# Kernel tuning notes

Measured on AMD Instinct MI355X. Metric: run time of the kernel, lower is better.

The kernel has to match this reference:

```python
import jax, jax.numpy as jnp
import numpy as np


def setup_inputs() -> dict:
    key = jax.random.key(0)
    k = jax.random.split(key, 5)
    C, Cb = 128, 64
    x = jax.random.normal(k[0], (8, C, 64, 64), dtype=jnp.float32)
    s_in = 1.0 / np.sqrt(C)
    s_b = 1.0 / np.sqrt(Cb)
    w_theta = jax.random.normal(k[1], (Cb, C), dtype=jnp.float32) * s_in
    w_phi = jax.random.normal(k[2], (Cb, C), dtype=jnp.float32) * s_in
    w_g = jax.random.normal(k[3], (Cb, C), dtype=jnp.float32) * s_in
    w_last = jax.random.normal(k[4], (C, Cb), dtype=jnp.float32) * s_b
    return {"x": x, "w_theta": w_theta, "w_phi": w_phi, "w_g": w_g, "w_last": w_last}


def reference(x, w_theta, w_phi, w_g, w_last):
    B, C, H, W = x.shape
    xf = x.reshape(B, C, H * W)            # [B, C, N]
    theta = jnp.einsum('kc,bcn->bkn', w_theta, xf)   # [B, Cb, N]
    phi = jnp.einsum('kc,bcn->bkn', w_phi, xf)       # [B, Cb, N]
    g = jnp.einsum('kc,bcn->bkn', w_g, xf)           # [B, Cb, N]
    # attention over spatial positions: [B, N, N]
    attn = jax.nn.softmax(jnp.einsum('bkn,bkm->bnm', theta, phi), axis=-1)
    y = jnp.einsum('bnm,bkm->bkn', attn, g)          # [B, Cb, N]
    out = jnp.einsum('ck,bkn->bcn', w_last, y).reshape(B, C, H, W)
    return out + x
```

## Files before the change

### kernel.cpp

```cpp
#include <hip/hip_runtime.h>
#include <stdint.h>

typedef _Float16 h8v __attribute__((ext_vector_type(8)));
typedef _Float16 h4v __attribute__((ext_vector_type(4)));
typedef float f4v __attribute__((ext_vector_type(4)));
typedef _Float16 f16;

#define NB 8
#define CC 128
#define CB 64
#define NN 4096
#define L2E 1.4426950408889634f

#define GLD(gp, lp) __builtin_amdgcn_global_load_lds( \
    (const __attribute__((address_space(1))) void*)(gp), \
    (__attribute__((address_space(3))) void*)(lp), 16, 0, 0)

#define WAITV2() asm volatile("s_waitcnt vmcnt(2)" ::: "memory")
#define WAITV0() asm volatile("s_waitcnt vmcnt(0)" ::: "memory")
#define WAITL0() asm volatile("s_waitcnt lgkmcnt(0)" ::: "memory")

__global__ __launch_bounds__(256) void pack_w(
    const float* __restrict__ wth, const float* __restrict__ wph,
    const float* __restrict__ wg,  const float* __restrict__ wl,
    f16* __restrict__ wthp, f16* __restrict__ wphp,
    f16* __restrict__ wgp,  f16* __restrict__ wlp)
{
    const int t = blockIdx.x * 256 + threadIdx.x;
    for (int i = t; i < 8192; i += 2048){
        const int j = i & 7, lane = (i >> 3) & 63, kc = (i >> 9) & 3, ks = i >> 11;
        const int row = ks * 16 + (lane & 15);
        const int col = kc * 32 + ((lane >> 4) & 3) * 8 + j;
        wthp[i] = (f16)(wth[row * CC + col] * L2E);
        wphp[i] = (f16)(wph[row * CC + col]);
        wgp [i] = (f16)(wg [row * CC + col]);
    }
    for (int i = t; i < 8192; i += 2048){
        const int j = i & 7, lane = (i >> 3) & 63, kc = (i >> 9) & 1, cs = i >> 10;
        const int row = cs * 16 + (lane & 15);
        const int col = kc * 32 + ((lane >> 4) & 3) * 8 + j;
        wlp[i] = (f16)(wl[row * CB + col]);
    }
}

__global__ __launch_bounds__(256) void proj_kernel(
    const float* __restrict__ x, const f16* __restrict__ wthp,
    const f16* __restrict__ wphp, const f16* __restrict__ wgp,
    f16* __restrict__ thetaT, f16* __restrict__ phiT, f16* __restrict__ gbuf)
{
    __shared__ __align__(16) f16 xT[64][136];
    __shared__ __align__(16) f16 rep[4][16 * 72];
    const int b  = blockIdx.x & 7;
    const int n0 = (blockIdx.x >> 3) << 6;
    const int t  = threadIdx.x;

    #pragma unroll
    for (int i = 0; i < 8; i++){
        int v  = t + 256 * i;
        int c  = v >> 4;
        int j0 = (v & 15) << 2;
        const f4v xv = *(const f4v*)&x[((size_t)(b * CC + c)) * NN + n0 + j0];
        #pragma unroll
        for (int jj = 0; jj < 4; jj++) xT[j0 + jj][c] = (f16)xv[jj];
    }
    __syncthreads();

    const int w = t >> 6, lane = t & 63, quad = lane >> 4, l15 = lane & 15;
    const int rrow = lane >> 3, rcol = (lane & 7) * 8;

    h8v bx[4];
    #pragma unroll
    for (int kc = 0; kc < 4; kc++)
        bx[kc] = *(const h8v*)&xT[w * 16 + l15][kc * 32 + quad * 8];

    #pragma unroll
    for (int m3 = 0; m3 < 2; m3++){
        const f16* WP = (m3 == 0) ? wthp : wphp;
        f16* OUT      = (m3 == 0) ? thetaT : phiT;
        for (int ks = 0; ks < 4; ks++){
            f4v acc = {0.f, 0.f, 0.f, 0.f};
            #pragma unroll
            for (int kc = 0; kc < 4; kc++){
                const h8v af = *(const h8v*)&WP[(ks * 4 + kc) * 512 + lane * 8];
                acc = __builtin_amdgcn_mfma_f32_16x16x32_f16(af, bx[kc], acc, 0, 0, 0);
            }
            h4v pv;
            #pragma unroll
            for (int r = 0; r < 4; r++) pv[r] = (f16)acc[r];
            *(h4v*)&rep[w][l15 * 72 + ks * 16 + quad * 4] = pv;
        }
        #pragma unroll
        for (int j = 0; j < 2; j++){
            const h8v vv = *(const h8v*)&rep[w][(rrow + 8 * j) * 72 + rcol];
            *(h8v*)&OUT[((size_t)(b * NN + n0 + w * 16 + rrow + 8 * j)) * CB + rcol] = vv;
        }
    }

    h8v bw[4];
    #pragma unroll
    for (int kc = 0; kc < 4; kc++)
        bw[kc] = *(const h8v*)&wgp[(w * 4 + kc) * 512 + lane * 8];
    for (int ns = 0; ns < 4; ns++){
        f4v acc = {0.f, 0.f, 0.f, 0.f};
        #pragma unroll
        for (int kc = 0; kc < 4; kc++){
            const h8v af = *(const h8v*)&xT[ns * 16 + l15][kc * 32 + quad * 8];
            acc = __builtin_amdgcn_mfma_f32_16x16x32_f16(af, bw[kc], acc, 0, 0, 0);
        }
        h4v pv;
        #pragma unroll
        for (int r = 0; r < 4; r++) pv[r] = (f16)acc[r];
        *(h4v*)&rep[w][l15 * 72 + ns * 16 + quad * 4] = pv;
    }
    #pragma unroll
    for (int j = 0; j < 2; j++){
        const h8v vv = *(const h8v*)&rep[w][(rrow + 8 * j) * 72 + rcol];
        *(h8v*)&gbuf[((size_t)(b * CB + w * 16 + rrow + 8 * j)) * NN + n0 + rcol] = vv;
    }
}

__global__ __launch_bounds__(512, 4) void attn_kernel(
    const f16* __restrict__ thetaT, const f16* __restrict__ phiT,
    const f16* __restrict__ gbuf, const f16* __restrict__ wlp,
    const float* __restrict__ x, float* __restrict__ out)
{
    __shared__ __align__(16) char SM[59392];
    f16*   const PH  = (f16*)SM;
    f16*   const GG  = (f16*)(SM + 24576);
    f16*   const PLD = (f16*)(SM + 49152);
    float* const MG  = (float*)SM;
    float* const ML  = (float*)(SM + 17408);
    float* const FO  = (float*)SM;
    f16*   const YY  = (f16*)(SM + 36864);

    const int b  = blockIdx.x & 7;
    const int q0 = (blockIdx.x >> 3) << 6;
    const int t  = threadIdx.x;
    const int w  = t >> 6;
    const int lane = t & 63, quad = lane >> 4, l15 = lane & 15;
    const int wq = w & 3;
    const int h  = w >> 2;
    const int n0 = q0 + wq * 16;

    const size_t trow = ((size_t)(b * NN + n0 + l15)) * CB;
    const h8v a0 = *(const h8v*)&thetaT[trow + quad * 8];
    const h8v a1 = *(const h8v*)&thetaT[trow + 32 + quad * 8];

    const int seg  = w * 2;
    const int tsel = seg >> 3;
    const int kind = (seg >> 2) & 1;
    const int qa   = seg & 3;
    const f16* sA;  const f16* sB;  size_t adv;
    if (kind == 0){
        const int row = qa * 8 + (lane >> 3);
        const int gr  = (lane & 7) ^ (lane >> 3);
        sA = phiT + ((size_t)(b * NN + tsel * 32 + row)) * CB + gr * 8;
        sB = sA + (size_t)8 * CB;
        adv = (size_t)64 * CB;
    } else {
        const int row = qa * 16 + (lane >> 2);
        const int gr  = (lane & 3) ^ ((lane >> 2) & 3);
        sA = gbuf + ((size_t)(b * CB + row)) * NN + tsel * 32 + gr * 8;
        sB = sA + (size_t)16 * NN;
        adv = 64;
    }
    f16* const dBase = (kind == 0) ? PH : GG;
    const int dOff = qa * 512;

    const int so0 = (quad ^ (l15 & 7)) * 8;
    const int so1 = so0 ^ 32;
    const int go  = (quad ^ (l15 & 3)) * 8;

    {
        f16* d0 = dBase + (0 + tsel) * 2048 + dOff;
        GLD(sA, d0);  GLD(sB, d0 + 512);
        f16* d1 = dBase + (2 + tsel) * 2048 + dOff;
        GLD(sA + adv, d1);  GLD(sB + adv, d1 + 512);
    }
    const f16* pA = sA + 2 * adv;
    const f16* pB = sB + 2 * adv;

    float mrun = -1e30f, lrun = 0.f;
    const f4v zf = {0.f, 0.f, 0.f, 0.f};
    f4v o[4];
    #pragma unroll
    for (int tt = 0; tt < 4; tt++) o[tt] = zf;

    f16* const PW = PLD + w * 640;

    int rc = 0;
    int rs = 2;
    for (int m = 0; m < 64; m++){
        if (m < 63) WAITV2(); else WAITV0();
        WAITL0();
        __builtin_amdgcn_s_barrier();
        asm volatile("" ::: "memory");
        if (m < 62){
            f16* d = dBase + (2 * rs + tsel) * 2048 + dOff;
            GLD(pA, d);  GLD(pB, d + 512);
            pA += adv;   pB += adv;
        }
        const int ct = 2 * rc + h;
        const f16* phc = PH + ct * 2048;
        const f16* ggc = GG + ct * 2048;

        f4v s[2];
        __builtin_amdgcn_s_setprio(1);
        #pragma unroll
        for (int tt = 0; tt < 2; tt++){
            const f16* pr = phc + (tt * 16 + l15) * 64;
            const h8v pb0 = *(const h8v*)(pr + so0);
            const h8v pb1 = *(const h8v*)(pr + so1);
            f4v sv = zf;
            sv = __builtin_amdgcn_mfma_f32_16x16x32_f16(pb0, a0, sv, 0, 0, 0);
            sv = __builtin_amdgcn_mfma_f32_16x16x32_f16(pb1, a1, sv, 0, 0, 0);
            s[tt] = sv;
        }
        __builtin_amdgcn_s_setprio(0);

        float smax = fmaxf(fmaxf(s[0][0], s[0][1]), fmaxf(s[0][2], s[0][3]));
        smax = fmaxf(smax, fmaxf(fmaxf(s[1][0], s[1][1]), fmaxf(s[1][2], s[1][3])));
        smax = fmaxf(smax, __shfl_xor(smax, 16));
        smax = fmaxf(smax, __shfl_xor(smax, 32));

        if (__any(smax - mrun > 8.f)){
            const float mn = fmaxf(mrun, smax);
            const float alpha = __builtin_amdgcn_exp2f(mrun - mn);
            mrun = mn;
            lrun *= alpha;
            #pragma unroll
            for (int tt = 0; tt < 4; tt++)
                #pragma unroll
                for (int r = 0; r < 4; r++)
                    o[tt][r] *= alpha;
        }

        float lsum = 0.f;
        #pragma unroll
        for (int tt = 0; tt < 2; tt++){
            h4v pv;
            #pragma unroll
            for (int r = 0; r < 4; r++){
                float p = __builtin_amdgcn_exp2f(s[tt][r] - mrun);
                lsum += p;
                pv[r] = (f16)p;
            }
            *(h4v*)&PW[l15 * 40 + tt * 16 + quad * 4] = pv;
        }
        lrun += lsum;

        const h8v pa = *(const h8v*)&PW[l15 * 40 + quad * 8];

        __builtin_amdgcn_s_setprio(1);
        #pragma unroll
        for (int tt2 = 0; tt2 < 4; tt2++){
            const h8v gb = *(const h8v*)(ggc + (tt2 * 16 + l15) * 32 + go);
            o[tt2] = __builtin_amdgcn_mfma_f32_16x16x32_f16(gb, pa, o[tt2], 0, 0, 0);
        }
        __builtin_amdgcn_s_setprio(0);

        rc = (rc == 2) ? 0 : rc + 1;
        rs = (rs == 2) ? 0 : rs + 1;
    }

    lrun += __shfl_xor(lrun, 16);
    lrun += __shfl_xor(lrun, 32);

    __syncthreads();

    if (h == 1){
        #pragma unroll
        for (int tt2 = 0; tt2 < 4; tt2++)
            *(f4v*)&MG[wq * 1088 + l15 * 68 + tt2 * 16 + quad * 4] = o[tt2];
        if (lane < 16){
            ML[wq * 32 + lane * 2 + 0] = mrun;
            ML[wq * 32 + lane * 2 + 1] = lrun;
        }
    }
    __syncthreads();

    if (h == 0){
        const float m4 = ML[wq * 32 + l15 * 2 + 0];
        const float l4 = ML[wq * 32 + l15 * 2 + 1];
        const float M  = fmaxf(mrun, m4);
        const float e0 = __builtin_amdgcn_exp2f(mrun - M);
        const float e1 = __builtin_amdgcn_exp2f(m4 - M);
        const float inv = 1.0f / (lrun * e0 + l4 * e1);
        #pragma unroll
        for (int tt2 = 0; tt2 < 4; tt2++){
            const f4v o4 = *(const f4v*)&MG[wq * 1088 + l15 * 68 + tt2 * 16 + quad * 4];
            h4v yv;
            #pragma unroll
            for (int r = 0; r < 4; r++)
                yv[r] = (f16)((o[tt2][r] * e0 + o4[r] * e1) * inv);
            *(h4v*)&YY[(wq * 16 + l15) * 72 + tt2 * 16 + quad * 4] = yv;
        }
    }
    __syncthreads();

    const h8v yB0 = *(const h8v*)&YY[(wq * 16 + l15) * 72 + quad * 8];
    const h8v yB1 = *(const h8v*)&YY[(wq * 16 + l15) * 72 + 32 + quad * 8];
    #pragma unroll
    for (int ci = 0; ci < 4; ci++){
        const int cs = h * 4 + ci;
        const h8v wa0 = *(const h8v*)&wlp[(cs * 2 + 0) * 512 + lane * 8];
        const h8v wa1 = *(const h8v*)&wlp[(cs * 2 + 1) * 512 + lane * 8];
        f4v acc = zf;
        acc = __builtin_amdgcn_mfma_f32_16x16x32_f16(wa0, yB0, acc, 0, 0, 0);
        acc = __builtin_amdgcn_mfma_f32_16x16x32_f16(wa1, yB1, acc, 0, 0, 0);
        #pragma unroll
        for (int r = 0; r < 4; r++)
            FO[(cs * 16 + quad * 4 + r) * 68 + wq * 16 + l15] = acc[r];
    }
    __syncthreads();

    #pragma unroll
    for (int i = 0; i < 4; i++){
        const int row = i * 32 + (t >> 4);
        const int nf  = (t & 15) * 4;
        const f4v v = *(const f4v*)&FO[row * 68 + nf];
        const size_t idx = ((size_t)(b * CC + row)) * NN + q0 + nf;
        const f4v xv = *(const f4v*)&x[idx];
        f4v ov;
        #pragma unroll
        for (int r = 0; r < 4; r++) ov[r] = v[r] + xv[r];
        *(f4v*)&out[idx] = ov;
    }
}

extern "C" void kernel_launch(void* const* d_in, const int* in_sizes, int n_in,
                              void* d_out, int out_size, void* d_ws, size_t ws_size,
                              hipStream_t stream)
{
    const float* x   = (const float*)d_in[0];
    const float* wth = (const float*)d_in[1];
    const float* wph = (const float*)d_in[2];
    const float* wg  = (const float*)d_in[3];
    const float* wl  = (const float*)d_in[4];
    float* out = (float*)d_out;

    f16* thetaT = (f16*)d_ws;
    f16* phiT   = thetaT + (size_t)NB * NN * CB;
    f16* gbuf   = phiT   + (size_t)NB * NN * CB;
    f16* wthp   = gbuf   + (size_t)NB * NN * CB;
    f16* wphp   = wthp + 8192;
    f16* wgp    = wphp + 8192;
    f16* wlp    = wgp  + 8192;

    pack_w<<<8, 256, 0, stream>>>(wth, wph, wg, wl, wthp, wphp, wgp, wlp);
    proj_kernel<<<NB * 64, 256, 0, stream>>>(x, wthp, wphp, wgp, thetaT, phiT, gbuf);
    attn_kernel<<<NB * 64, 512, 0, stream>>>(thetaT, phiT, gbuf, wlp, x, out);
}
```

Measured before the change: 150.7 us.

## Load g operand directly from global into registers and drop weight-pack kernel

The attention kernel no longer stages g tiles in shared memory. Each wave now loads its g MFMA operands directly from global memory into registers, and the shared-memory pipeline carries only phi in 128-key tiles, halving the loop trip count. The P·G MFMA is split into two halves so the P transpose buffer can be reused. The separate pack_w launch is removed, and weights are converted from fp32 to fp16 inline inside the projection and attention kernels. This trades shared-memory traffic and one launch for uncoalesced, strided global g loads whose latency is less hidden, plus redundant weight conversion in every block.

```diff
diff --git a/kernel.cpp b/kernel.cpp
--- a/kernel.cpp
+++ b/kernel.cpp
@@ -20,32 +20,9 @@
 #define WAITV0() asm volatile("s_waitcnt vmcnt(0)" ::: "memory")
 #define WAITL0() asm volatile("s_waitcnt lgkmcnt(0)" ::: "memory")
 
-__global__ __launch_bounds__(256) void pack_w(
-    const float* __restrict__ wth, const float* __restrict__ wph,
-    const float* __restrict__ wg,  const float* __restrict__ wl,
-    f16* __restrict__ wthp, f16* __restrict__ wphp,
-    f16* __restrict__ wgp,  f16* __restrict__ wlp)
-{
-    const int t = blockIdx.x * 256 + threadIdx.x;
-    for (int i = t; i < 8192; i += 2048){
-        const int j = i & 7, lane = (i >> 3) & 63, kc = (i >> 9) & 3, ks = i >> 11;
-        const int row = ks * 16 + (lane & 15);
-        const int col = kc * 32 + ((lane >> 4) & 3) * 8 + j;
-        wthp[i] = (f16)(wth[row * CC + col] * L2E);
-        wphp[i] = (f16)(wph[row * CC + col]);
-        wgp [i] = (f16)(wg [row * CC + col]);
-    }
-    for (int i = t; i < 8192; i += 2048){
-        const int j = i & 7, lane = (i >> 3) & 63, kc = (i >> 9) & 1, cs = i >> 10;
-        const int row = cs * 16 + (lane & 15);
-        const int col = kc * 32 + ((lane >> 4) & 3) * 8 + j;
-        wlp[i] = (f16)(wl[row * CB + col]);
-    }
-}
-
 __global__ __launch_bounds__(256) void proj_kernel(
-    const float* __restrict__ x, const f16* __restrict__ wthp,
-    const f16* __restrict__ wphp, const f16* __restrict__ wgp,
+    const float* __restrict__ x, const float* __restrict__ wth,
+    const float* __restrict__ wph, const float* __restrict__ wg,
     f16* __restrict__ thetaT, f16* __restrict__ phiT, f16* __restrict__ gbuf)
 {
     __shared__ __align__(16) f16 xT[64][136];
@@ -75,13 +52,22 @@
 
     #pragma unroll
     for (int m3 = 0; m3 < 2; m3++){
-        const f16* WP = (m3 == 0) ? wthp : wphp;
-        f16* OUT      = (m3 == 0) ? thetaT : phiT;
+        const float* WF = (m3 == 0) ? wth : wph;
+        const float sc = (m3 == 0) ? L2E : 1.0f;
+        f16* OUT       = (m3 == 0) ? thetaT : phiT;
         for (int ks = 0; ks < 4; ks++){
             f4v acc = {0.f, 0.f, 0.f, 0.f};
             #pragma unroll
             for (int kc = 0; kc < 4; kc++){
-                const h8v af = *(const h8v*)&WP[(ks * 4 + kc) * 512 + lane * 8];
+                const float* wr = WF + (ks * 16 + l15) * CC + kc * 32 + quad * 8;
+                const f4v wa = *(const f4v*)wr;
+                const f4v wb = *(const f4v*)(wr + 4);
+                h8v af;
+                #pragma unroll
+                for (int j = 0; j < 4; j++){
+                    af[j]     = (f16)(wa[j] * sc);
+                    af[4 + j] = (f16)(wb[j] * sc);
+                }
                 acc = __builtin_amdgcn_mfma_f32_16x16x32_f16(af, bx[kc], acc, 0, 0, 0);
             }
             h4v pv;
@@ -98,8 +84,16 @@
 
     h8v bw[4];
     #pragma unroll
-    for (int kc = 0; kc < 4; kc++)
-        bw[kc] = *(const h8v*)&wgp[(w * 4 + kc) * 512 + lane * 8];
+    for (int kc = 0; kc < 4; kc++){
+        const float* wr = wg + (w * 16 + l15) * CC + kc * 32 + quad * 8;
+        const f4v wa = *(const f4v*)wr;
+        const f4v wb = *(const f4v*)(wr + 4);
+        #pragma unroll
+        for (int j = 0; j < 4; j++){
+            bw[kc][j]     = (f16)wa[j];
+            bw[kc][4 + j] = (f16)wb[j];
+        }
+    }
     for (int ns = 0; ns < 4; ns++){
         f4v acc = {0.f, 0.f, 0.f, 0.f};
         #pragma unroll
@@ -121,12 +115,11 @@
 
 __global__ __launch_bounds__(512, 4) void attn_kernel(
     const f16* __restrict__ thetaT, const f16* __restrict__ phiT,
-    const f16* __restrict__ gbuf, const f16* __restrict__ wlp,
+    const f16* __restrict__ gbuf, const float* __restrict__ wl,
     const float* __restrict__ x, float* __restrict__ out)
 {
     __shared__ __align__(16) char SM[59392];
     f16*   const PH  = (f16*)SM;
-    f16*   const GG  = (f16*)(SM + 24576);
     f16*   const PLD = (f16*)(SM + 49152);
     float* const MG  = (float*)SM;
     float* const ML  = (float*)(SM + 17408);
@@ -146,39 +139,23 @@
     const h8v a0 = *(const h8v*)&thetaT[trow + quad * 8];
     const h8v a1 = *(const h8v*)&thetaT[trow + 32 + quad * 8];
 
-    const int seg  = w * 2;
-    const int tsel = seg >> 3;
-    const int kind = (seg >> 2) & 1;
-    const int qa   = seg & 3;
-    const f16* sA;  const f16* sB;  size_t adv;
-    if (kind == 0){
-        const int row = qa * 8 + (lane >> 3);
-        const int gr  = (lane & 7) ^ (lane >> 3);
-        sA = phiT + ((size_t)(b * NN + tsel * 32 + row)) * CB + gr * 8;
-        sB = sA + (size_t)8 * CB;
-        adv = (size_t)64 * CB;
-    } else {
-        const int row = qa * 16 + (lane >> 2);
-        const int gr  = (lane & 3) ^ ((lane >> 2) & 3);
-        sA = gbuf + ((size_t)(b * CB + row)) * NN + tsel * 32 + gr * 8;
-        sB = sA + (size_t)16 * NN;
-        adv = 64;
-    }
-    f16* const dBase = (kind == 0) ? PH : GG;
-    const int dOff = qa * 512;
+    const int r0 = t >> 3;
+    const int gr = (t & 7) ^ (r0 & 7);
+    const f16* pS = phiT + ((size_t)(b * NN + r0)) * CB + gr * 8;
+    const size_t SADV = (size_t)128 * CB;
 
     const int so0 = (quad ^ (l15 & 7)) * 8;
     const int so1 = so0 ^ 32;
-    const int go  = (quad ^ (l15 & 3)) * 8;
+
+    const f16* pgm = gbuf + ((size_t)(b * CB + l15)) * NN + 64 * h + quad * 8;
 
     {
-        f16* d0 = dBase + (0 + tsel) * 2048 + dOff;
-        GLD(sA, d0);  GLD(sB, d0 + 512);
-        f16* d1 = dBase + (2 + tsel) * 2048 + dOff;
-        GLD(sA + adv, d1);  GLD(sB + adv, d1 + 512);
-    }
-    const f16* pA = sA + 2 * adv;
-    const f16* pB = sB + 2 * adv;
+        GLD(pS,            PH + t * 8);
+        GLD(pS + 64 * CB,  PH + t * 8 + 4096);
+        GLD(pS + SADV,           PH + 8192 + t * 8);
+        GLD(pS + SADV + 64 * CB, PH + 8192 + t * 8 + 4096);
+        pS += 2 * SADV;
+    }
 
     float mrun = -1e30f, lrun = 0.f;
     const f4v zf = {0.f, 0.f, 0.f, 0.f};
@@ -190,24 +167,36 @@
 
     int rc = 0;
     int rs = 2;
-    for (int m = 0; m < 64; m++){
-        if (m < 63) WAITV2(); else WAITV0();
+    for (int m = 0; m < 32; m++){
+        if (m < 31) WAITV2(); else WAITV0();
         WAITL0();
         __builtin_amdgcn_s_barrier();
         asm volatile("" ::: "memory");
-        if (m < 62){
-            f16* d = dBase + (2 * rs + tsel) * 2048 + dOff;
-            GLD(pA, d);  GLD(pB, d + 512);
-            pA += adv;   pB += adv;
-        }
-        const int ct = 2 * rc + h;
-        const f16* phc = PH + ct * 2048;
-        const f16* ggc = GG + ct * 2048;
-
-        f4v s[2];
+
+        h8v g00, g01, g02, g03, g10, g11, g12, g13;
+        g00 = *(const h8v*)(pgm + (size_t)(0 * 16) * NN);
+        g01 = *(const h8v*)(pgm + (size_t)(1 * 16) * NN);
+        g02 = *(const h8v*)(pgm + (size_t)(2 * 16) * NN);
+        g03 = *(const h8v*)(pgm + (size_t)(3 * 16) * NN);
+        g10 = *(const h8v*)(pgm + (size_t)(0 * 16) * NN + 32);
+        g11 = *(const h8v*)(pgm + (size_t)(1 * 16) * NN + 32);
+        g12 = *(const h8v*)(pgm + (size_t)(2 * 16) * NN + 32);
+        g13 = *(const h8v*)(pgm + (size_t)(3 * 16) * NN + 32);
+        __builtin_amdgcn_sched_barrier(0);
+        if (m < 30){
+            f16* d = PH + rs * 8192 + t * 8;
+            GLD(pS, d);
+            GLD(pS + 64 * CB, d + 4096);
+            pS += SADV;
+        }
+        __builtin_amdgcn_sched_barrier(0);
+
+        const f16* phc = PH + rc * 8192 + h * 64 * 64;
+
+        f4v s[4];
         __builtin_amdgcn_s_setprio(1);
         #pragma unroll
-        for (int tt = 0; tt < 2; tt++){
+        for (int tt = 0; tt < 4; tt++){
             const f16* pr = phc + (tt * 16 + l15) * 64;
             const h8v pb0 = *(const h8v*)(pr + so0);
             const h8v pb1 = *(const h8v*)(pr + so1);
@@ -219,7 +208,9 @@
         __builtin_amdgcn_s_setprio(0);
 
         float smax = fmaxf(fmaxf(s[0][0], s[0][1]), fmaxf(s[0][2], s[0][3]));
-        smax = fmaxf(smax, fmaxf(fmaxf(s[1][0], s[1][1]), fmaxf(s[1][2], s[1][3])));
+        #pragma unroll
+        for (int tt = 1; tt < 4; tt++)
+            smax = fmaxf(smax, fmaxf(fmaxf(s[tt][0], s[tt][1]), fmaxf(s[tt][2], s[tt][3])));
         smax = fmaxf(smax, __shfl_xor(smax, 16));
         smax = fmaxf(smax, __shfl_xor(smax, 32));
 
@@ -236,8 +227,9 @@
         }
 
         float lsum = 0.f;
-        #pragma unroll
-        for (int tt = 0; tt < 2; tt++){
+        h4v pvh0, pvh1;
+        #pragma unroll
+        for (int tt = 0; tt < 4; tt++){
             h4v pv;
             #pragma unroll
             for (int r = 0; r < 4; r++){
@@ -245,20 +237,32 @@
                 lsum += p;
                 pv[r] = (f16)p;
             }
-            *(h4v*)&PW[l15 * 40 + tt * 16 + quad * 4] = pv;
+            if (tt == 0)      *(h4v*)&PW[l15 * 40 +      quad * 4] = pv;
+            else if (tt == 1) *(h4v*)&PW[l15 * 40 + 16 + quad * 4] = pv;
+            else if (tt == 2) pvh0 = pv;
+            else              pvh1 = pv;
         }
         lrun += lsum;
 
-        const h8v pa = *(const h8v*)&PW[l15 * 40 + quad * 8];
-
+        const h8v pa0 = *(const h8v*)&PW[l15 * 40 + quad * 8];
         __builtin_amdgcn_s_setprio(1);
-        #pragma unroll
-        for (int tt2 = 0; tt2 < 4; tt2++){
-            const h8v gb = *(const h8v*)(ggc + (tt2 * 16 + l15) * 32 + go);
-            o[tt2] = __builtin_amdgcn_mfma_f32_16x16x32_f16(gb, pa, o[tt2], 0, 0, 0);
-        }
+        o[0] = __builtin_amdgcn_mfma_f32_16x16x32_f16(g00, pa0, o[0], 0, 0, 0);
+        o[1] = __builtin_amdgcn_mfma_f32_16x16x32_f16(g01, pa0, o[1], 0, 0, 0);
+        o[2] = __builtin_amdgcn_mfma_f32_16x16x32_f16(g02, pa0, o[2], 0, 0, 0);
+        o[3] = __builtin_amdgcn_mfma_f32_16x16x32_f16(g03, pa0, o[3], 0, 0, 0);
         __builtin_amdgcn_s_setprio(0);
 
+        *(h4v*)&PW[l15 * 40 +      quad * 4] = pvh0;
+        *(h4v*)&PW[l15 * 40 + 16 + quad * 4] = pvh1;
+        const h8v pa1 = *(const h8v*)&PW[l15 * 40 + quad * 8];
+        __builtin_amdgcn_s_setprio(1);
+        o[0] = __builtin_amdgcn_mfma_f32_16x16x32_f16(g10, pa1, o[0], 0, 0, 0);
+        o[1] = __builtin_amdgcn_mfma_f32_16x16x32_f16(g11, pa1, o[1], 0, 0, 0);
+        o[2] = __builtin_amdgcn_mfma_f32_16x16x32_f16(g12, pa1, o[2], 0, 0, 0);
+        o[3] = __builtin_amdgcn_mfma_f32_16x16x32_f16(g13, pa1, o[3], 0, 0, 0);
+        __builtin_amdgcn_s_setprio(0);
+
+        pgm += 128;
         rc = (rc == 2) ? 0 : rc + 1;
         rs = (rs == 2) ? 0 : rs + 1;
     }
@@ -303,8 +307,19 @@
     #pragma unroll
     for (int ci = 0; ci < 4; ci++){
         const int cs = h * 4 + ci;
-        const h8v wa0 = *(const h8v*)&wlp[(cs * 2 + 0) * 512 + lane * 8];
-        const h8v wa1 = *(const h8v*)&wlp[(cs * 2 + 1) * 512 + lane * 8];
+        const float* wrow = wl + (cs * 16 + l15) * CB + quad * 8;
+        const f4v wA0 = *(const f4v*)(wrow);
+        const f4v wA1 = *(const f4v*)(wrow + 4);
+        const f4v wB0 = *(const f4v*)(wrow + 32);
+        const f4v wB1 = *(const f4v*)(wrow + 36);
+        h8v wa0, wa1;
+        #pragma unroll
+        for (int j = 0; j < 4; j++){
+            wa0[j]     = (f16)wA0[j];
+            wa0[4 + j] = (f16)wA1[j];
+            wa1[j]     = (f16)wB0[j];
+            wa1[4 + j] = (f16)wB1[j];
+        }
         f4v acc = zf;
         acc = __builtin_amdgcn_mfma_f32_16x16x32_f16(wa0, yB0, acc, 0, 0, 0);
         acc = __builtin_amdgcn_mfma_f32_16x16x32_f16(wa1, yB1, acc, 0, 0, 0);
@@ -342,12 +357,7 @@
     f16* thetaT = (f16*)d_ws;
     f16* phiT   = thetaT + (size_t)NB * NN * CB;
     f16* gbuf   = phiT   + (size_t)NB * NN * CB;
-    f16* wthp   = gbuf   + (size_t)NB * NN * CB;
-    f16* wphp   = wthp + 8192;
-    f16* wgp    = wphp + 8192;
-    f16* wlp    = wgp  + 8192;
-
-    pack_w<<<8, 256, 0, stream>>>(wth, wph, wg, wl, wthp, wphp, wgp, wlp);
-    proj_kernel<<<NB * 64, 256, 0, stream>>>(x, wthp, wphp, wgp, thetaT, phiT, gbuf);
-    attn_kernel<<<NB * 64, 512, 0, stream>>>(thetaT, phiT, gbuf, wlp, x, out);
+
+    proj_kernel<<<NB * 64, 256, 0, stream>>>(x, wth, wph, wg, thetaT, phiT, gbuf);
+    attn_kernel<<<NB * 64, 512, 0, stream>>>(thetaT, phiT, gbuf, wl, x, out);
 }
```

Result: slower. 233.9 us (+55.2%).
